# Kernel optimization log

Hardware: AMD Instinct MI355X
Metric: run time of the kernel (lower is better)

Reference implementation:

```python
import jax, jax.numpy as jnp
import numpy as np

H = 128   # render_height
W = 128   # render_width
N = 128   # primitives per frame (from view(B,128,12,2))
K = 12    # control points / polygon vertices per primitive
SOFT = 0.01  # fallback_softness of DiffRasterizer


def setup_inputs() -> dict:
    key = jax.random.key(0)
    k1, k2, k3, k4, k5 = jax.random.split(key, 5)
    T, B = 192, 1
    # state = [3072 control-point coords in [0,1] | 128 aliveness logits]
    trajectory = jax.random.uniform(k1, (T, B, N * K * 2 + N), dtype=jnp.float32)
    colors = jax.random.uniform(k2, (B, N, 3), dtype=jnp.float32)
    alpha = jax.random.uniform(k3, (N,), dtype=jnp.float32)
    z = jax.random.normal(k4, (N,), dtype=jnp.float32)
    csg = jax.random.randint(k5, (N,), 0, 2) > 0
    return {"trajectory": trajectory, "colors": colors, "alpha": alpha, "z": z, "csg": csg}


def _raster(P, c, alpha, alive, z, csg, gx, gy):
    """Soft differentiable rasterizer (fallback path).
    P: [N,K,2] polygon control points in [0,1]; c: [N,3]; alpha/alive/z: [N]; csg: [N] bool.
    Coverage: product of per-edge half-plane sigmoids (soft convex polygon),
    orientation-corrected via shoelace sign. Composited back-to-front by z;
    CSG-subtract primitives erase (occlude) without contributing color.
    """
    v0 = P                                   # [N,K,2]
    v1 = jnp.roll(P, -1, axis=1)             # [N,K,2]
    e = v1 - v0                              # edge vectors
    area2 = jnp.sum(v0[..., 0] * v1[..., 1] - v1[..., 0] * v0[..., 1], axis=1)  # [N]
    orient = jax.lax.stop_gradient(jnp.sign(area2))[:, None]                    # [N,1]
    # signed edge tests for every pixel: [H,W,N,K]
    s = e[..., 0] * (gy[:, :, None, None] - v0[..., 1]) \
      - e[..., 1] * (gx[:, :, None, None] - v0[..., 0])
    cov = jnp.prod(jax.nn.sigmoid(s * orient / SOFT), axis=-1)  # [H,W,N]
    a = cov * alpha * jax.nn.sigmoid(alive)                     # per-primitive alpha
    order = jnp.argsort(z)                                      # back-to-front
    a = a[..., order]
    c = c[order]
    sub = csg[order].astype(a.dtype)
    one_m = 1.0 - a
    # exclusive reverse cumulative transmittance T_i = prod_{j>i}(1 - a_j)
    t_acc = jnp.flip(jnp.cumprod(jnp.flip(one_m, -1), -1), -1)
    t_excl = jnp.concatenate([t_acc[..., 1:], jnp.ones_like(t_acc[..., :1])], -1)
    w = a * t_excl * (1.0 - sub)             # [H,W,N]
    return jnp.einsum('hwn,nc->hwc', w, c)   # [H,W,3]


def reference(trajectory, colors, alpha, z, csg):
    T, B, _ = trajectory.shape
    ys = (jnp.arange(H, dtype=jnp.float32) + 0.5) / H
    xs = (jnp.arange(W, dtype=jnp.float32) + 0.5) / W
    gy, gx = jnp.meshgrid(ys, xs, indexing='ij')  # [H,W]

    def frame(state_t):  # state_t: [B, 3200]
        P = state_t[:, :N * K * 2].reshape(B, N, K, 2)
        alive = state_t[:, N * K * 2:].reshape(B, N)
        return jax.vmap(lambda Pb, cb, ab: _raster(Pb, cb, alpha, ab, z, csg, gx, gy))(P, colors, alive)

    video = jax.lax.map(jax.checkpoint(frame), trajectory)  # [T,B,H,W,3]
    return jnp.transpose(video, (1, 0, 2, 3, 4))            # [B,T,H,W,3]
```

## Files before the change

kernel.cpp:

```cpp
#include <hip/hip_runtime.h>


#define HH 128
#define WW 128
#define NN 128
#define KK 12
#define STPB 1024
#define RTPB 256
#define STATE_SZ (NN * KK * 2 + NN)
#define CULL_U 15.0f
#define COEF_STRIDE 40
#define PQ_STRIDE 18

typedef float f2 __attribute__((ext_vector_type(2)));

__global__ __launch_bounds__(STPB) void setup_kernel(
    const float* __restrict__ traj,
    const float* __restrict__ colors,
    const float* __restrict__ alpha,
    const float* __restrict__ zval,
    const void*  __restrict__ csg_raw,
    float* __restrict__ g_coef,
    int* __restrict__ g_cnt,
    unsigned char* __restrict__ g_list)
{
    __shared__ __align__(16) float s_coef[NN][COEF_STRIDE];
    __shared__ __align__(16) float2 s_pq[NN][PQ_STRIDE];
    __shared__ float s_state[STATE_SZ];
    __shared__ float s_orient[NN];
    __shared__ float s_z[NN];
    __shared__ int   s_slot2prim[NN];
    __shared__ int   s_npos[NN], s_nneg[NN];
    __shared__ unsigned long long s_qbits[HH][4][2];
    __shared__ unsigned char s_list[4 * (HH / 2)][NN];
    __shared__ int s_cnt[4 * (HH / 2)];
    __shared__ int s_mode;

    const int frame = blockIdx.x;
    const int tid   = threadIdx.x;
    const float* st = traj + (size_t)frame * STATE_SZ;

    for (int i = tid; i < STATE_SZ; i += STPB) s_state[i] = st[i];
    if (tid < NN) { s_z[tid] = zval[tid]; s_npos[tid] = 0; s_nneg[tid] = 0; }
    if (tid < 64) {
        unsigned w = (tid < 32) ? ((const unsigned*)csg_raw)[tid] : 0u;
        unsigned long long anyw = __ballot(w > 1u);
        unsigned long long anyb = __ballot((w & 0xFEFEFEFEu) != 0u);
        if (tid == 0) s_mode = (anyw == 0ull) ? 0 : ((anyb == 0ull) ? 1 : 2);
    }
    __syncthreads();

    if (tid < NN) {
        const int n = tid;
        float area2 = 0.f;
        #pragma unroll
        for (int k = 0; k < KK; k++) {
            int k1 = (k + 1) % KK;
            float v0x = s_state[(n * KK + k)  * 2 + 0];
            float v0y = s_state[(n * KK + k)  * 2 + 1];
            float v1x = s_state[(n * KK + k1) * 2 + 0];
            float v1y = s_state[(n * KK + k1) * 2 + 1];
            area2 += v0x * v1y - v1x * v0y;
        }
        float orient = (area2 > 0.f) ? 1.f : ((area2 < 0.f) ? -1.f : 0.f);
        s_orient[n] = orient;

        float alive = s_state[NN * KK * 2 + n];
        float g = alpha[n] / (1.f + __expf(-alive));

        float zn = s_z[n];
        int rank = 0;
        #pragma unroll 8
        for (int j = 0; j < NN; j++) {
            float zj = s_z[j];
            rank += (zj < zn || (zj == zn && j < n)) ? 1 : 0;
        }
        int slot = (NN - 1) - rank;
        s_slot2prim[slot] = n;

        int mode = s_mode;
        int sub;
        if (mode == 0)      sub = ((const int*)csg_raw)[n] != 0;
        else if (mode == 1) sub = ((const unsigned char*)csg_raw)[n] != 0;
        else                sub = ((const float*)csg_raw)[n] != 0.f;
        float cs = sub ? 0.f : 1.f;
        s_coef[slot][36] = g;
        s_coef[slot][37] = colors[n * 3 + 0] * cs;
        s_coef[slot][38] = colors[n * 3 + 1] * cs;
        s_coef[slot][39] = colors[n * 3 + 2] * cs;
    }
    __syncthreads();

    const float QSCALE = 100.0f * 1.4426950408889634f;
    for (int idx = tid; idx < NN * KK; idx += STPB) {
        int slot = idx / KK;
        int k    = idx - slot * KK;
        int n    = s_slot2prim[slot];
        int k1   = (k + 1) % KK;
        float v0x = s_state[(n * KK + k)  * 2 + 0];
        float v0y = s_state[(n * KK + k)  * 2 + 1];
        float v1x = s_state[(n * KK + k1) * 2 + 0];
        float v1y = s_state[(n * KK + k1) * 2 + 1];
        float ex = v1x - v0x, ey = v1y - v0y;
        float q  = -s_orient[n] * QSCALE;
        s_coef[slot][0  + k] = q * ex;
        s_coef[slot][12 + k] = -q * ey;
        s_coef[slot][24 + k] = -q * (ex * v0y - ey * v0x);
    }
    __syncthreads();

    const float SLACK = 0.01f;
    for (int idx = tid; idx < NN * KK; idx += STPB) {
        int slot = idx / KK;
        int k    = idx - slot * KK;
        (void)k;
        float A = s_coef[slot][idx - slot * KK];
        float B = s_coef[slot][12 + (idx - slot * KK)];
        float C = s_coef[slot][24 + (idx - slot * KK)];
        float rcpB = __builtin_amdgcn_rcpf(B);
        float Praw = (CULL_U - C) * rcpB;
        float Qraw = -A * rcpB;
        if (B > 0.f) {
            int i = atomicAdd(&s_npos[slot], 1);
            s_pq[slot][i] = make_float2(Qraw, Praw + SLACK);
        } else if (B < 0.f) {
            int i = atomicAdd(&s_nneg[slot], 1);
            s_pq[slot][(KK - 1) - i] = make_float2(-Qraw, -Praw + SLACK);
        } else {
            int i = atomicAdd(&s_nneg[slot], 1);
            s_pq[slot][(KK - 1) - i] = make_float2(0.f, 1e30f);
        }
    }
    __syncthreads();

    const float GX_LO = 0.5f / WW;
    const float GX_HI = (WW - 0.5f) / WW;
    for (int j = 0; j < (HH * NN) / STPB; j++) {
        int idx = j * STPB + tid;
        int r = idx >> 7, s = idx & (NN - 1);
        float gyr = (r + 0.5f) * (1.0f / HH);
        int npos = s_npos[s];
        const float4* pq4 = (const float4*)&s_pq[s][0];
        float y1 = 1e30f, y2 = 1e30f;
        #pragma unroll
        for (int h = 0; h < KK / 2; h++) {
            float4 v = pq4[h];
            int k0 = 2 * h, k1 = 2 * h + 1;
            float t0 = fmaf(v.x, gyr, v.y);
            float t1 = fmaf(v.z, gyr, v.w);
            bool p0 = k0 < npos, p1 = k1 < npos;
            y1 = fminf(y1, p0 ? t0 : 1e30f);
            y2 = fminf(y2, p0 ? 1e30f : t0);
            y1 = fminf(y1, p1 ? t1 : 1e30f);
            y2 = fminf(y2, p1 ? 1e30f : t1);
        }
        float xhi = fminf(y1, GX_HI);
        float xlo = fmaxf(-y2, GX_LO);
        bool ne = (xlo <= xhi);
        #pragma unroll
        for (int q = 0; q < 4; q++) {
            float qlo = (q * 32 + 0.5f) * (1.0f / WW);
            float qhi = (q * 32 + 31.5f) * (1.0f / WW);
            unsigned long long m = __ballot(ne && (xlo <= qhi) && (xhi >= qlo));
            if ((tid & 63) == 0) s_qbits[r][q][(s >= 64) ? 1 : 0] = m;
        }
    }
    __syncthreads();

    {
        int wvS = tid >> 6;
        int ln  = tid & 63;
        for (int it = 0; it < 16; it++) {
            int t = wvS * 16 + it;
            int rp = t >> 2, qq = t & 3;
            unsigned long long b0 = s_qbits[2 * rp][qq][0] | s_qbits[2 * rp + 1][qq][0];
            unsigned long long b1 = s_qbits[2 * rp][qq][1] | s_qbits[2 * rp + 1][qq][1];
            int c0 = __popcll(b0);
            int p0 = __builtin_amdgcn_mbcnt_hi((unsigned)(b0 >> 32),
                     __builtin_amdgcn_mbcnt_lo((unsigned)b0, 0));
            int p1 = __builtin_amdgcn_mbcnt_hi((unsigned)(b1 >> 32),
                     __builtin_amdgcn_mbcnt_lo((unsigned)b1, 0));
            if ((b0 >> ln) & 1ull) s_list[t][p0]      = (unsigned char)ln;
            if ((b1 >> ln) & 1ull) s_list[t][c0 + p1] = (unsigned char)(64 + ln);
            if (ln == 0) s_cnt[t] = c0 + __popcll(b1);
        }
    }
    __syncthreads();

    {
        float* dstc = g_coef + (size_t)frame * (NN * COEF_STRIDE);
        const float* srcc = &s_coef[0][0];
        for (int i = tid; i < NN * COEF_STRIDE; i += STPB) dstc[i] = srcc[i];
        if (tid < 256) g_cnt[frame * 256 + tid] = s_cnt[tid];
        unsigned int* dstl = (unsigned int*)(g_list + (size_t)frame * (256 * NN));
        const unsigned int* srcl = (const unsigned int*)&s_list[0][0];
        for (int i = tid; i < (256 * NN) / 4; i += STPB) dstl[i] = srcl[i];
    }
}

struct F3 { float x, y, z; };

__global__ __launch_bounds__(RTPB) void raster_kernel(
    const float* __restrict__ g_coef,
    const int* __restrict__ g_cnt,
    const unsigned char* __restrict__ g_list,
    float* __restrict__ out)
{
    __shared__ unsigned char s_wlist[4][NN];

    const int tid   = threadIdx.x;
    const int wv    = __builtin_amdgcn_readfirstlane(tid >> 6);
    const int lane  = tid & 63;
    const int frame = blockIdx.y;
    const int tile  = blockIdx.x * 4 + wv;
    const int rp    = tile >> 2;
    const int q     = tile & 3;

    const unsigned char* lst = g_list + ((size_t)frame * 256 + tile) * NN;
    if (lane < NN / 4) {
        ((unsigned int*)&s_wlist[wv][0])[lane] = ((const unsigned int*)lst)[lane];
    }
    const int cnt = g_cnt[frame * 256 + tile];

    const int lx  = lane & 31, ly = lane >> 5;
    const int px  = q * 32 + lx;
    const int row = rp * 2 + ly;
    const float gy = (row + 0.5f) * (1.0f / HH);
    const float gx = (px  + 0.5f) * (1.0f / WW);
    const f2 gy2 = {gy, gy};
    const f2 gx2 = {gx, gx};
    const f2 lo2 = {-100.f, -100.f};

    const float* cfr = g_coef + (size_t)frame * (NN * COEF_STRIDE);

    float Tt = 1.f, rr = 0.f, gg = 0.f, bb = 0.f;
    if (cnt > 0) {
        int sl_n = __builtin_amdgcn_readfirstlane((int)s_wlist[wv][0]);
        const float* cfn = cfr + sl_n * COEF_STRIDE;
        f2 An[6], Bn[6], Cn[6]; float4 gcn;
        #pragma unroll
        for (int j = 0; j < 6; j++) {
            An[j] = ((const f2*)(cfn     ))[j];
            Bn[j] = ((const f2*)(cfn + 12))[j];
            Cn[j] = ((const f2*)(cfn + 24))[j];
        }
        gcn = *(const float4*)(cfn + 36);

        for (int i = 0; i < cnt; i++) {
            f2 A[6], B[6], C[6]; float4 gc = gcn;
            #pragma unroll
            for (int j = 0; j < 6; j++) { A[j] = An[j]; B[j] = Bn[j]; C[j] = Cn[j]; }

            int inx = (i + 1 < cnt) ? (i + 1) : i;
            sl_n = __builtin_amdgcn_readfirstlane((int)s_wlist[wv][inx]);
            cfn = cfr + sl_n * COEF_STRIDE;
            #pragma unroll
            for (int j = 0; j < 6; j++) {
                An[j] = ((const f2*)(cfn     ))[j];
                Bn[j] = ((const f2*)(cfn + 12))[j];
                Cn[j] = ((const f2*)(cfn + 24))[j];
            }
            gcn = *(const float4*)(cfn + 36);

            f2 qv = {1.f, 1.f};
            #pragma unroll
            for (int j = 0; j < 6; j++) {
                f2 u = __builtin_elementwise_fma(B[j], gx2,
                         __builtin_elementwise_fma(A[j], gy2, C[j]));
                u = __builtin_elementwise_max(u, lo2);
                f2 e;
                e.x = __builtin_amdgcn_exp2f(u.x);
                e.y = __builtin_amdgcn_exp2f(u.y);
                qv = __builtin_elementwise_fma(qv, e, qv);
            }
            float cov = __builtin_amdgcn_rcpf(qv.x * qv.y);

            float a = cov * gc.x;
            float w = a * Tt;
            rr = fmaf(w, gc.y, rr);
            gg = fmaf(w, gc.z, gg);
            bb = fmaf(w, gc.w, bb);
            Tt = fmaf(-a, Tt, Tt);

            if (!__any(Tt > 2e-3f)) break;
        }
    }

    size_t o = ((size_t)frame * (HH * WW) + (size_t)row * WW + px) * 3;
    *(F3*)(out + o) = F3{rr, gg, bb};
}

extern "C" void kernel_launch(void* const* d_in, const int* in_sizes, int n_in,
                              void* d_out, int out_size, void* d_ws, size_t ws_size,
                              hipStream_t stream) {
    const float* traj   = (const float*)d_in[0];
    const float* colors = (const float*)d_in[1];
    const float* alpha  = (const float*)d_in[2];
    const float* zval   = (const float*)d_in[3];
    const void*  csg    = d_in[4];
    float* out = (float*)d_out;

    const int T = in_sizes[0] / STATE_SZ;

    size_t coef_sz = (size_t)T * NN * COEF_STRIDE * sizeof(float);
    size_t cnt_sz  = (size_t)T * 256 * sizeof(int);
    float* g_coef = (float*)d_ws;
    int*   g_cnt  = (int*)((char*)d_ws + coef_sz);
    unsigned char* g_list = (unsigned char*)d_ws + coef_sz + cnt_sz;

    setup_kernel<<<T, STPB, 0, stream>>>(traj, colors, alpha, zval, csg,
                                         g_coef, g_cnt, g_list);
    dim3 grid(256 / 4, T);
    raster_kernel<<<grid, RTPB, 0, stream>>>(g_coef, g_cnt, g_list, out);
}
```

Baseline: 228.0 us.

## Split setup into per-frame and per-band kernels; double-buffer raster coefficient loads

The single 1024-thread per-frame setup kernel becomes two kernels. setup_a computes edge coefficients and per-edge bounds with 256 threads per frame. setup_b builds the tile primitive lists over a grid of 8 row bands × T frames and writes them straight to global memory, which is meant to raise parallelism and cut the large LDS footprint. The raster kernel drops its LDS list copy, reads packed list bytes directly with readfirstlane, and uses a manually double-buffered float4 prefetch of primitive coefficients. In exchange there is an extra launch and a round-trip of pq data through global memory.

```diff
diff --git a/kernel.cpp b/kernel.cpp
--- a/kernel.cpp
+++ b/kernel.cpp
@@ -5,42 +5,43 @@
 #define WW 128
 #define NN 128
 #define KK 12
-#define STPB 1024
+#define SAPB 256
+#define SBPB 256
 #define RTPB 256
 #define STATE_SZ (NN * KK * 2 + NN)
 #define CULL_U 15.0f
 #define COEF_STRIDE 40
-#define PQ_STRIDE 18
+#define PQ_LSTR 18
 
 typedef float f2 __attribute__((ext_vector_type(2)));
 
-__global__ __launch_bounds__(STPB) void setup_kernel(
+static __device__ inline f2 mk2(float a, float b) { f2 r; r.x = a; r.y = b; return r; }
+
+__global__ __launch_bounds__(SAPB) void setup_a(
     const float* __restrict__ traj,
     const float* __restrict__ colors,
     const float* __restrict__ alpha,
     const float* __restrict__ zval,
     const void*  __restrict__ csg_raw,
     float* __restrict__ g_coef,
-    int* __restrict__ g_cnt,
-    unsigned char* __restrict__ g_list)
+    float2* __restrict__ g_pq,
+    int* __restrict__ g_npos)
 {
+    __shared__ float s_state[STATE_SZ];
     __shared__ __align__(16) float s_coef[NN][COEF_STRIDE];
-    __shared__ __align__(16) float2 s_pq[NN][PQ_STRIDE];
-    __shared__ float s_state[STATE_SZ];
+    __shared__ __align__(16) float2 s_pq[NN][KK];
     __shared__ float s_orient[NN];
     __shared__ float s_z[NN];
     __shared__ int   s_slot2prim[NN];
     __shared__ int   s_npos[NN], s_nneg[NN];
-    __shared__ unsigned long long s_qbits[HH][4][2];
-    __shared__ unsigned char s_list[4 * (HH / 2)][NN];
-    __shared__ int s_cnt[4 * (HH / 2)];
-    __shared__ int s_mode;
+    __shared__ int   s_mode;
 
     const int frame = blockIdx.x;
     const int tid   = threadIdx.x;
     const float* st = traj + (size_t)frame * STATE_SZ;
 
-    for (int i = tid; i < STATE_SZ; i += STPB) s_state[i] = st[i];
+    for (int i = tid; i < STATE_SZ / 4; i += SAPB)
+        ((float4*)s_state)[i] = ((const float4*)st)[i];
     if (tid < NN) { s_z[tid] = zval[tid]; s_npos[tid] = 0; s_nneg[tid] = 0; }
     if (tid < 64) {
         unsigned w = (tid < 32) ? ((const unsigned*)csg_raw)[tid] : 0u;
@@ -92,7 +93,7 @@
     __syncthreads();
 
     const float QSCALE = 100.0f * 1.4426950408889634f;
-    for (int idx = tid; idx < NN * KK; idx += STPB) {
+    for (int idx = tid; idx < NN * KK; idx += SAPB) {
         int slot = idx / KK;
         int k    = idx - slot * KK;
         int n    = s_slot2prim[slot];
@@ -110,13 +111,12 @@
     __syncthreads();
 
     const float SLACK = 0.01f;
-    for (int idx = tid; idx < NN * KK; idx += STPB) {
+    for (int idx = tid; idx < NN * KK; idx += SAPB) {
         int slot = idx / KK;
         int k    = idx - slot * KK;
-        (void)k;
-        float A = s_coef[slot][idx - slot * KK];
-        float B = s_coef[slot][12 + (idx - slot * KK)];
-        float C = s_coef[slot][24 + (idx - slot * KK)];
+        float A = s_coef[slot][k];
+        float B = s_coef[slot][12 + k];
+        float C = s_coef[slot][24 + k];
         float rcpB = __builtin_amdgcn_rcpf(B);
         float Praw = (CULL_U - C) * rcpB;
         float Qraw = -A * rcpB;
@@ -133,14 +133,48 @@
     }
     __syncthreads();
 
+    {
+        float4* dstc = (float4*)(g_coef + (size_t)frame * (NN * COEF_STRIDE));
+        const float4* srcc = (const float4*)&s_coef[0][0];
+        for (int i = tid; i < (NN * COEF_STRIDE) / 4; i += SAPB) dstc[i] = srcc[i];
+        float4* dstp = (float4*)(g_pq + (size_t)frame * (NN * KK));
+        const float4* srcp = (const float4*)&s_pq[0][0];
+        for (int i = tid; i < (NN * KK) / 2; i += SAPB) dstp[i] = srcp[i];
+        if (tid < NN) g_npos[frame * NN + tid] = s_npos[tid];
+    }
+}
+
+__global__ __launch_bounds__(SBPB) void setup_b(
+    const float2* __restrict__ g_pq,
+    const int* __restrict__ g_npos,
+    int* __restrict__ g_cnt,
+    unsigned char* __restrict__ g_list)
+{
+    __shared__ __align__(16) float2 s_pqp[NN][PQ_LSTR];
+    __shared__ int s_np[NN];
+    __shared__ unsigned long long s_qb[16][4][2];
+
+    const int band  = blockIdx.x;
+    const int frame = blockIdx.y;
+    const int tid   = threadIdx.x;
+
+    const float2* pqf = g_pq + (size_t)frame * (NN * KK);
+    for (int i = tid; i < NN * KK; i += SBPB) {
+        int slot = i / KK, k = i - slot * KK;
+        s_pqp[slot][k] = pqf[i];
+    }
+    if (tid < NN) s_np[tid] = g_npos[frame * NN + tid];
+    __syncthreads();
+
     const float GX_LO = 0.5f / WW;
     const float GX_HI = (WW - 0.5f) / WW;
-    for (int j = 0; j < (HH * NN) / STPB; j++) {
-        int idx = j * STPB + tid;
-        int r = idx >> 7, s = idx & (NN - 1);
-        float gyr = (r + 0.5f) * (1.0f / HH);
-        int npos = s_npos[s];
-        const float4* pq4 = (const float4*)&s_pq[s][0];
+    for (int j = 0; j < (16 * NN) / SBPB; j++) {
+        int idx = j * SBPB + tid;
+        int rl = idx >> 7, s = idx & (NN - 1);
+        int row = band * 16 + rl;
+        float gyr = (row + 0.5f) * (1.0f / HH);
+        int npos = s_np[s];
+        const float4* pq4 = (const float4*)&s_pqp[s][0];
         float y1 = 1e30f, y2 = 1e30f;
         #pragma unroll
         for (int h = 0; h < KK / 2; h++) {
@@ -162,7 +196,7 @@
             float qlo = (q * 32 + 0.5f) * (1.0f / WW);
             float qhi = (q * 32 + 31.5f) * (1.0f / WW);
             unsigned long long m = __ballot(ne && (xlo <= qhi) && (xhi >= qlo));
-            if ((tid & 63) == 0) s_qbits[r][q][(s >= 64) ? 1 : 0] = m;
+            if ((tid & 63) == 0) s_qb[rl][q][(s >= 64) ? 1 : 0] = m;
         }
     }
     __syncthreads();
@@ -170,35 +204,55 @@
     {
         int wvS = tid >> 6;
         int ln  = tid & 63;
-        for (int it = 0; it < 16; it++) {
-            int t = wvS * 16 + it;
-            int rp = t >> 2, qq = t & 3;
-            unsigned long long b0 = s_qbits[2 * rp][qq][0] | s_qbits[2 * rp + 1][qq][0];
-            unsigned long long b1 = s_qbits[2 * rp][qq][1] | s_qbits[2 * rp + 1][qq][1];
+        for (int it = 0; it < 8; it++) {
+            int tl  = wvS * 8 + it;
+            int rpl = tl >> 2, qq = tl & 3;
+            unsigned long long b0 = s_qb[2 * rpl][qq][0] | s_qb[2 * rpl + 1][qq][0];
+            unsigned long long b1 = s_qb[2 * rpl][qq][1] | s_qb[2 * rpl + 1][qq][1];
+            int gtile = band * 32 + tl;
+            unsigned char* dst = g_list + ((size_t)frame * 256 + gtile) * NN;
             int c0 = __popcll(b0);
             int p0 = __builtin_amdgcn_mbcnt_hi((unsigned)(b0 >> 32),
                      __builtin_amdgcn_mbcnt_lo((unsigned)b0, 0));
             int p1 = __builtin_amdgcn_mbcnt_hi((unsigned)(b1 >> 32),
                      __builtin_amdgcn_mbcnt_lo((unsigned)b1, 0));
-            if ((b0 >> ln) & 1ull) s_list[t][p0]      = (unsigned char)ln;
-            if ((b1 >> ln) & 1ull) s_list[t][c0 + p1] = (unsigned char)(64 + ln);
-            if (ln == 0) s_cnt[t] = c0 + __popcll(b1);
-        }
-    }
-    __syncthreads();
-
-    {
-        float* dstc = g_coef + (size_t)frame * (NN * COEF_STRIDE);
-        const float* srcc = &s_coef[0][0];
-        for (int i = tid; i < NN * COEF_STRIDE; i += STPB) dstc[i] = srcc[i];
-        if (tid < 256) g_cnt[frame * 256 + tid] = s_cnt[tid];
-        unsigned int* dstl = (unsigned int*)(g_list + (size_t)frame * (256 * NN));
-        const unsigned int* srcl = (const unsigned int*)&s_list[0][0];
-        for (int i = tid; i < (256 * NN) / 4; i += STPB) dstl[i] = srcl[i];
+            if ((b0 >> ln) & 1ull) dst[p0]      = (unsigned char)ln;
+            if ((b1 >> ln) & 1ull) dst[c0 + p1] = (unsigned char)(64 + ln);
+            if (ln == 0) g_cnt[frame * 256 + gtile] = c0 + __popcll(b1);
+        }
     }
 }
 
 struct F3 { float x, y, z; };
+
+#define LOADQ(P, Q0,Q1,Q2,Q3,Q4,Q5,Q6,Q7,Q8,Q9)                         \
+    { const float4* c4_ = (const float4*)(P);                           \
+      asm("" : "+v"(c4_));                                              \
+      Q0 = c4_[0]; Q1 = c4_[1]; Q2 = c4_[2]; Q3 = c4_[3]; Q4 = c4_[4];  \
+      Q5 = c4_[5]; Q6 = c4_[6]; Q7 = c4_[7]; Q8 = c4_[8]; Q9 = c4_[9]; }
+
+#define EDGE2(Af, Bf, Cf)                                               \
+    { f2 u = __builtin_elementwise_fma(Bf, gx2,                         \
+              __builtin_elementwise_fma(Af, gy2, Cf));                  \
+      u = __builtin_elementwise_max(u, lo2);                            \
+      f2 e; e.x = __builtin_amdgcn_exp2f(u.x);                          \
+      e.y = __builtin_amdgcn_exp2f(u.y);                                \
+      qv = __builtin_elementwise_fma(qv, e, qv); }
+
+#define COMPUTE(Q0,Q1,Q2,Q3,Q4,Q5,Q6,Q7,Q8,Q9)                          \
+    { f2 qv = mk2(1.f, 1.f);                                            \
+      EDGE2(mk2(Q0.x,Q0.y), mk2(Q3.x,Q3.y), mk2(Q6.x,Q6.y));            \
+      EDGE2(mk2(Q0.z,Q0.w), mk2(Q3.z,Q3.w), mk2(Q6.z,Q6.w));            \
+      EDGE2(mk2(Q1.x,Q1.y), mk2(Q4.x,Q4.y), mk2(Q7.x,Q7.y));            \
+      EDGE2(mk2(Q1.z,Q1.w), mk2(Q4.z,Q4.w), mk2(Q7.z,Q7.w));            \
+      EDGE2(mk2(Q2.x,Q2.y), mk2(Q5.x,Q5.y), mk2(Q8.x,Q8.y));            \
+      EDGE2(mk2(Q2.z,Q2.w), mk2(Q5.z,Q5.w), mk2(Q8.z,Q8.w));            \
+      float cov = __builtin_amdgcn_rcpf(qv.x * qv.y);                   \
+      float a = cov * Q9.x;                                             \
+      float w = a * Tt;                                                 \
+      rr = fmaf(w, Q9.y, rr); gg = fmaf(w, Q9.z, gg);                   \
+      bb = fmaf(w, Q9.w, bb);                                           \
+      Tt = fmaf(-a, Tt, Tt); }
 
 __global__ __launch_bounds__(RTPB) void raster_kernel(
     const float* __restrict__ g_coef,
@@ -206,10 +260,8 @@
     const unsigned char* __restrict__ g_list,
     float* __restrict__ out)
 {
-    __shared__ unsigned char s_wlist[4][NN];
-
     const int tid   = threadIdx.x;
-    const int wv    = __builtin_amdgcn_readfirstlane(tid >> 6);
+    const int wv    = tid >> 6;
     const int lane  = tid & 63;
     const int frame = blockIdx.y;
     const int tile  = blockIdx.x * 4 + wv;
@@ -217,9 +269,7 @@
     const int q     = tile & 3;
 
     const unsigned char* lst = g_list + ((size_t)frame * 256 + tile) * NN;
-    if (lane < NN / 4) {
-        ((unsigned int*)&s_wlist[wv][0])[lane] = ((const unsigned int*)lst)[lane];
-    }
+    const unsigned* lw = (const unsigned*)lst;
     const int cnt = g_cnt[frame * 256 + tile];
 
     const int lx  = lane & 31, ly = lane >> 5;
@@ -227,62 +277,40 @@
     const int row = rp * 2 + ly;
     const float gy = (row + 0.5f) * (1.0f / HH);
     const float gx = (px  + 0.5f) * (1.0f / WW);
-    const f2 gy2 = {gy, gy};
-    const f2 gx2 = {gx, gx};
-    const f2 lo2 = {-100.f, -100.f};
+    const f2 gy2 = mk2(gy, gy);
+    const f2 gx2 = mk2(gx, gx);
+    const f2 lo2 = mk2(-100.f, -100.f);
 
     const float* cfr = g_coef + (size_t)frame * (NN * COEF_STRIDE);
 
     float Tt = 1.f, rr = 0.f, gg = 0.f, bb = 0.f;
     if (cnt > 0) {
-        int sl_n = __builtin_amdgcn_readfirstlane((int)s_wlist[wv][0]);
-        const float* cfn = cfr + sl_n * COEF_STRIDE;
-        f2 An[6], Bn[6], Cn[6]; float4 gcn;
-        #pragma unroll
-        for (int j = 0; j < 6; j++) {
-            An[j] = ((const f2*)(cfn     ))[j];
-            Bn[j] = ((const f2*)(cfn + 12))[j];
-            Cn[j] = ((const f2*)(cfn + 24))[j];
-        }
-        gcn = *(const float4*)(cfn + 36);
-
-        for (int i = 0; i < cnt; i++) {
-            f2 A[6], B[6], C[6]; float4 gc = gcn;
-            #pragma unroll
-            for (int j = 0; j < 6; j++) { A[j] = An[j]; B[j] = Bn[j]; C[j] = Cn[j]; }
-
-            int inx = (i + 1 < cnt) ? (i + 1) : i;
-            sl_n = __builtin_amdgcn_readfirstlane((int)s_wlist[wv][inx]);
-            cfn = cfr + sl_n * COEF_STRIDE;
-            #pragma unroll
-            for (int j = 0; j < 6; j++) {
-                An[j] = ((const f2*)(cfn     ))[j];
-                Bn[j] = ((const f2*)(cfn + 12))[j];
-                Cn[j] = ((const f2*)(cfn + 24))[j];
+        float4 A0,A1,A2,A3,A4,A5,A6,A7,A8,A9;
+        float4 B0,B1,B2,B3,B4,B5,B6,B7,B8,B9;
+        unsigned w0 = (unsigned)__builtin_amdgcn_readfirstlane((int)lw[0]);
+        int sC = (int)(w0 & 0xFFu);
+        int sN = (cnt > 1) ? (int)((w0 >> 8) & 0xFFu) : sC;
+        LOADQ(cfr + sC * COEF_STRIDE, A0,A1,A2,A3,A4,A5,A6,A7,A8,A9);
+        int i = 0;
+        for (;;) {
+            {
+                int ip2 = (i + 2 < cnt) ? i + 2 : cnt - 1;
+                unsigned wrd = lw[ip2 >> 2];
+                LOADQ(cfr + sN * COEF_STRIDE, B0,B1,B2,B3,B4,B5,B6,B7,B8,B9);
+                COMPUTE(A0,A1,A2,A3,A4,A5,A6,A7,A8,A9);
+                sN = (int)((((unsigned)__builtin_amdgcn_readfirstlane((int)wrd))
+                            >> ((ip2 & 3) * 8)) & 0xFFu);
             }
-            gcn = *(const float4*)(cfn + 36);
-
-            f2 qv = {1.f, 1.f};
-            #pragma unroll
-            for (int j = 0; j < 6; j++) {
-                f2 u = __builtin_elementwise_fma(B[j], gx2,
-                         __builtin_elementwise_fma(A[j], gy2, C[j]));
-                u = __builtin_elementwise_max(u, lo2);
-                f2 e;
-                e.x = __builtin_amdgcn_exp2f(u.x);
-                e.y = __builtin_amdgcn_exp2f(u.y);
-                qv = __builtin_elementwise_fma(qv, e, qv);
+            if (++i >= cnt || !__any(Tt > 2e-3f)) break;
+            {
+                int ip2 = (i + 2 < cnt) ? i + 2 : cnt - 1;
+                unsigned wrd = lw[ip2 >> 2];
+                LOADQ(cfr + sN * COEF_STRIDE, A0,A1,A2,A3,A4,A5,A6,A7,A8,A9);
+                COMPUTE(B0,B1,B2,B3,B4,B5,B6,B7,B8,B9);
+                sN = (int)((((unsigned)__builtin_amdgcn_readfirstlane((int)wrd))
+                            >> ((ip2 & 3) * 8)) & 0xFFu);
             }
-            float cov = __builtin_amdgcn_rcpf(qv.x * qv.y);
-
-            float a = cov * gc.x;
-            float w = a * Tt;
-            rr = fmaf(w, gc.y, rr);
-            gg = fmaf(w, gc.z, gg);
-            bb = fmaf(w, gc.w, bb);
-            Tt = fmaf(-a, Tt, Tt);
-
-            if (!__any(Tt > 2e-3f)) break;
+            if (++i >= cnt || !__any(Tt > 2e-3f)) break;
         }
     }
 
@@ -304,12 +332,18 @@
 
     size_t coef_sz = (size_t)T * NN * COEF_STRIDE * sizeof(float);
     size_t cnt_sz  = (size_t)T * 256 * sizeof(int);
-    float* g_coef = (float*)d_ws;
-    int*   g_cnt  = (int*)((char*)d_ws + coef_sz);
-    unsigned char* g_list = (unsigned char*)d_ws + coef_sz + cnt_sz;
-
-    setup_kernel<<<T, STPB, 0, stream>>>(traj, colors, alpha, zval, csg,
-                                         g_coef, g_cnt, g_list);
+    size_t list_sz = (size_t)T * 256 * NN;
+    size_t pq_sz   = (size_t)T * NN * KK * sizeof(float2);
+    char* p = (char*)d_ws;
+    float*         g_coef = (float*)p;          p += coef_sz;
+    int*           g_cnt  = (int*)p;            p += cnt_sz;
+    unsigned char* g_list = (unsigned char*)p;  p += list_sz;
+    float2*        g_pq   = (float2*)p;         p += pq_sz;
+    int*           g_npos = (int*)p;
+
+    setup_a<<<T, SAPB, 0, stream>>>(traj, colors, alpha, zval, csg,
+                                    g_coef, g_pq, g_npos);
+    setup_b<<<dim3(8, T), SBPB, 0, stream>>>(g_pq, g_npos, g_cnt, g_list);
     dim3 grid(256 / 4, T);
     raster_kernel<<<grid, RTPB, 0, stream>>>(g_coef, g_cnt, g_list, out);
 }
```

New measurement: 307.0 us. 1.35x slower.
